# Performance work log

Measured on AMD Instinct MI355X. Metric: run time of the kernel, lower is better.

The kernel has to match this reference:

```python
import jax, jax.numpy as jnp
import numpy as np

B, L, DIM = 16, 4096, 512
N_FFT, HOP, WIN = 1024, 256, 1024
PAD = (WIN - HOP) // 2  # 'same' padding trim
OUT_DIM = N_FFT + 2


def hann_window(win):
    n = jnp.arange(win, dtype=jnp.float32)
    return 0.5 - 0.5 * jnp.cos(2.0 * jnp.pi * n / win)


def setup_inputs() -> dict:
    key = jax.random.key(0)
    k1, k2 = jax.random.split(key)
    x = jax.random.normal(k1, (B, L, DIM), dtype=jnp.float32)
    W = jax.random.normal(k2, (OUT_DIM, DIM), dtype=jnp.float32) * 0.02
    b = jnp.zeros((OUT_DIM,), dtype=jnp.float32)
    return {"x": x, "W": W, "b": b}


def _istft(S):
    # S: (B, N_FFT//2+1, T) complex rfft spectrum
    T = S.shape[-1]
    frames = jnp.fft.irfft(S, n=N_FFT, axis=1)
    window = hann_window(WIN)
    frames = frames * window[None, :, None]
    out_len = (T - 1) * HOP + WIN
    idx = jnp.arange(T)[:, None] * HOP + jnp.arange(WIN)[None, :]
    fr = frames.transpose(0, 2, 1)
    y = jnp.zeros((fr.shape[0], out_len), fr.dtype).at[:, idx].add(fr)
    env = jnp.zeros((out_len,), fr.dtype).at[idx].add(
        jnp.broadcast_to(window * window, idx.shape))
    y = y[:, PAD:out_len - PAD]
    env = env[PAD:out_len - PAD]
    return y / env


def reference(x, W, b):
    # Linear projection: (B, L, DIM) -> (B, L, N_FFT+2)
    h = jnp.einsum('bld,od->blo', x, W) + b
    h = h.transpose(0, 2, 1)                              # (B, N_FFT+2, L)
    mag, p = jnp.split(h, 2, axis=1)                      # each (B, N_FFT//2+1, L)
    mag = jnp.minimum(jnp.exp(mag), 100.0)                # exp + clip(max=100)
    S = mag * jax.lax.complex(jnp.cos(p), jnp.sin(p))
    return _istft(S)                                      # (B, L*HOP)
```

## Files before the change

kernel.cpp:

```cpp
#include <hip/hip_runtime.h>
#include <hip/hip_bf16.h>
#include <math.h>

#define BATCH   16
#define TFRM    4096
#define DIM     512
#define NFFT    1024
#define HOP     256
#define PADC    384
#define MROWS   (BATCH*TFRM)
#define OUTLEN  1048576
#define TWO_PI_OVER_N 0.006135923151542565f
#define INV_TWO_PI    0.15915494309189535f

typedef __bf16 bf16x8 __attribute__((ext_vector_type(8)));
typedef float  f32x4  __attribute__((ext_vector_type(4)));

__device__ __forceinline__ ushort f2bf(float f) {
  union { float f; unsigned u; } v; v.f = f;
  unsigned u = v.u;
  unsigned r = (u + 0x7FFFu + ((u >> 16) & 1u)) >> 16;
  return (ushort)r;
}
__device__ __forceinline__ float bf2f(ushort h) {
  union { unsigned u; float f; } v; v.u = ((unsigned)h) << 16;
  return v.f;
}
__device__ __forceinline__ float fast_sin(float x) { return __builtin_amdgcn_sinf(x * INV_TWO_PI); }
__device__ __forceinline__ float fast_cos(float x) { return __builtin_amdgcn_cosf(x * INV_TWO_PI); }
__device__ __forceinline__ float fast_exp(float x) { return __builtin_amdgcn_exp2f(x * 1.4426950408889634f); }

#define BAR() do { asm volatile("" ::: "memory"); __builtin_amdgcn_s_barrier(); \
                   asm volatile("" ::: "memory"); } while (0)

__global__ void k_prep_x(const float* __restrict__ x, const float* __restrict__ W,
                         const float* __restrict__ bias,
                         ushort* __restrict__ xbf, float* __restrict__ s512) {
  const int row  = blockIdx.x * 4 + (threadIdx.x >> 6);
  const int lane = threadIdx.x & 63;
  const float* xr = x + (size_t)row * DIM + lane * 8;
  float4 v0 = *(const float4*)xr;
  float4 v1 = *(const float4*)(xr + 4);
  ushort4 u0, u1;
  u0.x = f2bf(v0.x); u0.y = f2bf(v0.y); u0.z = f2bf(v0.z); u0.w = f2bf(v0.w);
  u1.x = f2bf(v1.x); u1.y = f2bf(v1.y); u1.z = f2bf(v1.z); u1.w = f2bf(v1.w);
  ushort* xo = xbf + (size_t)row * DIM + lane * 8;
  *(ushort4*)xo = u0;
  *(ushort4*)(xo + 4) = u1;
  const float* w0 = W + 512 * DIM + lane * 8;
  const float* w1 = W + 1025 * DIM + lane * 8;
  float4 a0 = *(const float4*)w0, a1 = *(const float4*)(w0 + 4);
  float4 b0 = *(const float4*)w1, b1 = *(const float4*)(w1 + 4);
  float sm = v0.x*a0.x + v0.y*a0.y + v0.z*a0.z + v0.w*a0.w
           + v1.x*a1.x + v1.y*a1.y + v1.z*a1.z + v1.w*a1.w;
  float sp = v0.x*b0.x + v0.y*b0.y + v0.z*b0.z + v0.w*b0.w
           + v1.x*b1.x + v1.y*b1.y + v1.z*b1.z + v1.w*b1.w;
#pragma unroll
  for (int off = 32; off; off >>= 1) {
    sm += __shfl_down(sm, off);
    sp += __shfl_down(sp, off);
  }
  if (lane == 0) {
    float mag = fminf(fast_exp(sm + bias[512]), 100.0f);
    s512[row] = mag * fast_cos(sp + bias[1025]) * (1.0f / 1024.0f);
  }
}

__global__ void k_prep_w(const float* __restrict__ W, ushort* __restrict__ o) {
  int i = blockIdx.x * 256 + threadIdx.x;
  int r = i >> 9;
  int c = i & 511;
  int orig = (r >> 1) + (r & 1) * 513;
  o[i] = f2bf(W[orig * DIM + c]);
}

__global__ void k_basis(ushort* __restrict__ basE, ushort* __restrict__ basO) {
  int r = blockIdx.x;
  int n = r + 1;
  for (int k = threadIdx.x; k < 512; k += 256) {
    float e, o;
    if (k == 0) { e = 1.0f / 1024.0f; o = 0.0f; }
    else {
      int ph = (k * n) & 1023;
      float ang = (float)ph * TWO_PI_OVER_N;
      e = 2.0f * cosf(ang) * (1.0f / 1024.0f);
      o = 2.0f * sinf(ang) * (1.0f / 1024.0f);
    }
    basE[r * 512 + k] = f2bf(e);
    basO[r * 512 + k] = f2bf(o);
  }
}

template<int EPI>
__global__ __launch_bounds__(512, 2) void k_gemm(const ushort* A, const ushort* A2, int lda,
                                                 const ushort* Bt, const ushort* Bt2, int ldb,
                                                 ushort* C, ushort* C2, int ldc,
                                                 int nbn, int NK, int nsplit,
                                                 const float* __restrict__ bias) {
  __shared__ ushort lds[4][2][8192];
  const int tid  = threadIdx.x;
  const int cpx  = gridDim.x >> 3;
  int bid = (blockIdx.x & 7) * cpx + (blockIdx.x >> 3);
  if (nsplit > 0 && bid >= nsplit) { A = A2; Bt = Bt2; C = C2; bid -= nsplit; }
  const int bm   = bid / nbn;
  const int bn   = bid - bm * nbn;
  const int lane = tid & 63;
  const int wv   = tid >> 6;
  const int wr   = (wv >> 2) * 128;
  const int wc   = (wv & 3) * 64;
  const int fr   = lane & 15;
  const int gq   = lane >> 4;

  const int swz  = ((tid & 3) ^ ((tid >> 3) & 3)) << 3;
  const ushort* gA0 = A  + (size_t)(bm * 256 + (tid >> 2)) * lda + swz;
  const ushort* gA1 = gA0 + (size_t)128 * lda;
  const ushort* gB0 = Bt + (size_t)(bn * 256 + (tid >> 2)) * ldb + swz;
  const ushort* gB1 = gB0 + (size_t)128 * ldb;
  const int lofs = (tid & 448) * 8;

  auto stageA = [&](int S) {
    ushort* d = &lds[S & 3][0][0];
    __builtin_amdgcn_global_load_lds((const __attribute__((address_space(1))) void*)(gA0 + S * 32),
        (__attribute__((address_space(3))) void*)(d + lofs), 16, 0, 0);
    __builtin_amdgcn_global_load_lds((const __attribute__((address_space(1))) void*)(gA1 + S * 32),
        (__attribute__((address_space(3))) void*)(d + 4096 + lofs), 16, 0, 0);
  };
  auto stageB = [&](int S) {
    ushort* d = &lds[S & 3][1][0];
    __builtin_amdgcn_global_load_lds((const __attribute__((address_space(1))) void*)(gB0 + S * 32),
        (__attribute__((address_space(3))) void*)(d + lofs), 16, 0, 0);
    __builtin_amdgcn_global_load_lds((const __attribute__((address_space(1))) void*)(gB1 + S * 32),
        (__attribute__((address_space(3))) void*)(d + 4096 + lofs), 16, 0, 0);
  };
  auto frag = [&](const ushort* lb, int row) -> bf16x8 {
    return *(const bf16x8*)(lb + row * 32 + ((gq ^ ((row >> 1) & 3)) << 3));
  };

  f32x4 acc[8][4] = {};
  bf16x8 bF[4];

  auto phase = [&](int t, int mq, int stg, bool stgA, int wn) {
    const ushort* lA = &lds[t & 3][0][0];
    const ushort* lB = &lds[t & 3][1][0];
    bf16x8 aQ[4];
#pragma unroll
    for (int m = 0; m < 4; ++m) aQ[m] = frag(lA, wr + mq * 64 + m * 16 + fr);
    if (mq == 0) {
#pragma unroll
      for (int n = 0; n < 4; ++n) bF[n] = frag(lB, wc + n * 16 + fr);
    }
    if (stg >= 0) { if (stgA) stageA(stg); else stageB(stg); }
    BAR();
    asm volatile("s_waitcnt lgkmcnt(0)" ::: "memory");
    __builtin_amdgcn_s_setprio(1);
#pragma unroll
    for (int m = 0; m < 4; ++m)
#pragma unroll
      for (int n = 0; n < 4; ++n)
        acc[mq * 4 + m][n] =
            __builtin_amdgcn_mfma_f32_16x16x32_bf16(aQ[m], bF[n], acc[mq * 4 + m][n], 0, 0, 0);
    __builtin_amdgcn_s_setprio(0);
    if (wn == 8)      asm volatile("s_waitcnt vmcnt(8)" ::: "memory");
    else if (wn == 4) asm volatile("s_waitcnt vmcnt(4)" ::: "memory");
    else if (wn == 0) asm volatile("s_waitcnt vmcnt(0)" ::: "memory");
    BAR();
  };

  stageA(0); stageB(0); stageA(1); stageB(1); stageA(2); stageB(2);
  asm volatile("s_waitcnt vmcnt(8)" ::: "memory");
  BAR();

  const int NIT = NK >> 1;
  int j = 0;
  for (; j < NIT - 2; ++j) {
    const int u = 2 * j;
    phase(u,     0, u + 3, true,  -1);
    phase(u,     1, u + 3, false,  8);
    phase(u + 1, 0, u + 4, true,  -1);
    phase(u + 1, 1, u + 4, false,  8);
  }
  {
    const int u = 2 * j;
    phase(u,     0, u + 3, true,  -1);
    phase(u,     1, u + 3, false,  8);
    phase(u + 1, 0, -1,    true,  -1);
    phase(u + 1, 1, -1,    false,  4);
    ++j;
  }
  {
    const int u = 2 * j;
    phase(u,     0, -1, true,  -1);
    phase(u,     1, -1, false,  0);
    phase(u + 1, 0, -1, true,  -1);
    phase(u + 1, 1, -1, false, -1);
  }

  const int r0 = bm * 256 + wr + (gq << 2);
  const int c0 = bn * 256 + wc + fr;
#pragma unroll
  for (int m = 0; m < 8; ++m) {
    if constexpr (EPI == 0) {
#pragma unroll
      for (int j2 = 0; j2 < 4; ++j2) {
        size_t ro = (size_t)(r0 + m * 16 + j2) * ldc + c0;
#pragma unroll
        for (int n = 0; n < 4; ++n)
          C[ro + n * 16] = f2bf(acc[m][n][j2]);
      }
    } else {
#pragma unroll
      for (int n = 0; n < 4; ++n) {
        const int col = c0 + n * 16;
        const int kk  = col >> 1;
        const bool isPhase = (col & 1);
        const float bs = bias[isPhase ? 513 + kk : kk];
        ushort* dst = (isPhase ? C2 : C);
#pragma unroll
        for (int j2 = 0; j2 < 4; ++j2) {
          float v = acc[m][n][j2] + bs;
          float pv = __shfl_xor(v, 1);
          float hm = isPhase ? pv : v;
          float hp = isPhase ? v : pv;
          float mag = fminf(fast_exp(hm), 100.0f);
          float outv = isPhase ? mag * fast_sin(hp) : mag * fast_cos(hp);
          dst[(size_t)(r0 + m * 16 + j2) * ldc + kk] = f2bf(outv);
        }
      }
    }
  }
}

__global__ void k_oa(const ushort* __restrict__ E, const ushort* __restrict__ O,
                     const float* __restrict__ s512, float* __restrict__ out) {
  int u = blockIdx.x * 256 + threadIdx.x;
  int b  = u >> 20;
  int sp = u & (OUTLEN - 1);
  int s  = sp + PADC;
  int t0 = s >> 8;
  int nb = s & 255;
  float acc = 0.0f;
  bool interior = (t0 >= 3) && (t0 < TFRM);
  float env = interior ? 1.5f : 0.0f;
#pragma unroll
  for (int q = 0; q < 4; ++q) {
    int t = t0 - q;
    if (t >= 0 && t < TFRM) {
      int n = nb + (q << 8);
      float w = 0.5f - 0.5f * __builtin_amdgcn_cosf((float)n * (1.0f / 1024.0f));
      if (!interior) env += w * w;
      if (n > 0) {
        size_t base = (((size_t)(b << 12) + t) << 9);
        float sv = s512[(b << 12) + t];
        float par = (n & 1) ? -sv : sv;
        float d;
        if (n <= 512) {
          int idx = n - 1;
          d = bf2f(E[base + idx]) - bf2f(O[base + idx]) + par;
        } else {
          int idx = 1023 - n;
          d = bf2f(E[base + idx]) + bf2f(O[base + idx]) + par;
        }
        acc += w * d;
      }
    }
  }
  out[u] = acc / env;
}

extern "C" void kernel_launch(void* const* d_in, const int* in_sizes, int n_in,
                              void* d_out, int out_size, void* d_ws, size_t ws_size,
                              hipStream_t stream) {
  const float* x    = (const float*)d_in[0];
  const float* W    = (const float*)d_in[1];
  const float* bias = (const float*)d_in[2];
  float* out = (float*)d_out;
  char* ws = (char*)d_ws;

  ushort* xbf  = (ushort*)(ws + 0);
  ushort* Ebuf = (ushort*)(ws + 0);
  ushort* h_a  = (ushort*)(ws + 67108864);
  ushort* h_b  = (ushort*)(ws + 134217728);
  ushort* Obuf = (ushort*)(ws + 201326592);
  ushort* Wp   = (ushort*)(ws + 268435456);
  ushort* basE = (ushort*)(ws + 269484032);
  ushort* basO = (ushort*)(ws + 270008320);
  float*  s512 = (float*) (ws + 270532608);

  k_prep_x<<<MROWS / 4, 256, 0, stream>>>(x, W, bias, xbf, s512);
  k_prep_w<<<(1024 * 512) / 256, 256, 0, stream>>>(W, Wp);
  k_basis<<<512, 256, 0, stream>>>(basE, basO);

  k_gemm<1><<<1024, 512, 0, stream>>>(xbf, nullptr, DIM, Wp, nullptr, DIM,
                                      h_a, h_b, 512, 4, 16, 0, bias);

  k_gemm<0><<<1024, 512, 0, stream>>>(h_a, h_b, 512, basE, basO, 512,
                                      Ebuf, Obuf, 512, 2, 16, 512, nullptr);

  k_oa<<<(BATCH * OUTLEN) / 256, 256, 0, stream>>>(Ebuf, Obuf, s512, out);
}
```

Before: 330.8 us.

## Shrink GEMM tiles to 128x128 double-buffer, fold Nyquist term into GEMM, vectorize overlap-add

Replaces the 256x256 four-stage pipelined GEMM (512 threads, phased MFMA schedule with setprio) with a simpler 128x128 tile, 256-thread, double-buffered loop that syncs every K step. The second GEMM epilogue now adds the Nyquist/parity term from s512 and writes into a padded row stride (520) shifted by one column, so the overlap-add kernel no longer reads s512. The overlap-add kernel handles four output samples per thread with ushort4 loads and float4 stores. The simpler GEMM loses the deeper prefetch and larger tile reuse, which may cost MFMA throughput. In exchange it gains more blocks and simpler indexing.

Result: faster. 314.0 us (-5.1%).

```diff
diff --git a/kernel.cpp b/kernel.cpp
--- a/kernel.cpp
+++ b/kernel.cpp
@@ -10,6 +10,7 @@
 #define PADC    384
 #define MROWS   (BATCH*TFRM)
 #define OUTLEN  1048576
+#define ESTR    520
 #define TWO_PI_OVER_N 0.006135923151542565f
 #define INV_TWO_PI    0.15915494309189535f
 
@@ -29,9 +30,6 @@
 __device__ __forceinline__ float fast_sin(float x) { return __builtin_amdgcn_sinf(x * INV_TWO_PI); }
 __device__ __forceinline__ float fast_cos(float x) { return __builtin_amdgcn_cosf(x * INV_TWO_PI); }
 __device__ __forceinline__ float fast_exp(float x) { return __builtin_amdgcn_exp2f(x * 1.4426950408889634f); }
-
-#define BAR() do { asm volatile("" ::: "memory"); __builtin_amdgcn_s_barrier(); \
-                   asm volatile("" ::: "memory"); } while (0)
 
 __global__ void k_prep_x(const float* __restrict__ x, const float* __restrict__ W,
                          const float* __restrict__ bias,
@@ -92,120 +90,88 @@
 }
 
 template<int EPI>
-__global__ __launch_bounds__(512, 2) void k_gemm(const ushort* A, const ushort* A2, int lda,
-                                                 const ushort* Bt, const ushort* Bt2, int ldb,
-                                                 ushort* C, ushort* C2, int ldc,
-                                                 int nbn, int NK, int nsplit,
-                                                 const float* __restrict__ bias) {
-  __shared__ ushort lds[4][2][8192];
+__global__ __launch_bounds__(256) void k_gemm(const ushort* A, const ushort* A2, int lda,
+                                              const ushort* Bt, const ushort* Bt2, int ldb,
+                                              ushort* C, ushort* C2, int ldc,
+                                              int nbn, int NK, int nsplit,
+                                              const float* __restrict__ bias,
+                                              const float* __restrict__ s512) {
+  __shared__ __align__(16) ushort lds[2][2][128 * 32];
   const int tid  = threadIdx.x;
   const int cpx  = gridDim.x >> 3;
-  int bid = (blockIdx.x & 7) * cpx + (blockIdx.x >> 3);
-  if (nsplit > 0 && bid >= nsplit) { A = A2; Bt = Bt2; C = C2; bid -= nsplit; }
+  int bid  = (blockIdx.x & 7) * cpx + (blockIdx.x >> 3);
+  bool second = false;
+  if (nsplit > 0 && bid >= nsplit) { second = true; A = A2; Bt = Bt2; C = C2; bid -= nsplit; }
   const int bm   = bid / nbn;
   const int bn   = bid - bm * nbn;
   const int lane = tid & 63;
   const int wv   = tid >> 6;
-  const int wr   = (wv >> 2) * 128;
-  const int wc   = (wv & 3) * 64;
-  const int fr   = lane & 15;
-  const int gq   = lane >> 4;
-
-  const int swz  = ((tid & 3) ^ ((tid >> 3) & 3)) << 3;
-  const ushort* gA0 = A  + (size_t)(bm * 256 + (tid >> 2)) * lda + swz;
-  const ushort* gA1 = gA0 + (size_t)128 * lda;
-  const ushort* gB0 = Bt + (size_t)(bn * 256 + (tid >> 2)) * ldb + swz;
-  const ushort* gB1 = gB0 + (size_t)128 * ldb;
-  const int lofs = (tid & 448) * 8;
-
-  auto stageA = [&](int S) {
-    ushort* d = &lds[S & 3][0][0];
-    __builtin_amdgcn_global_load_lds((const __attribute__((address_space(1))) void*)(gA0 + S * 32),
-        (__attribute__((address_space(3))) void*)(d + lofs), 16, 0, 0);
-    __builtin_amdgcn_global_load_lds((const __attribute__((address_space(1))) void*)(gA1 + S * 32),
-        (__attribute__((address_space(3))) void*)(d + 4096 + lofs), 16, 0, 0);
+  const int wr   = (wv >> 1) * 64;
+  const int wc   = (wv & 1) * 64;
+  const int lr   = lane & 15;
+  const int gx   = ((lane >> 4) ^ (lane & 3)) << 3;
+
+  f32x4 acc[4][4] = {};
+
+  const int swz = ((tid & 3) ^ ((tid >> 2) & 3)) << 3;
+  auto stage = [&](const ushort* __restrict__ g, int ld, int row0, int k0, ushort* l) {
+#pragma unroll
+    for (int p = 0; p < 2; ++p) {
+      int i = tid + p * 256;
+      const ushort* gp = g + (size_t)(row0 + (i >> 2)) * ld + k0 + swz;
+      ushort* lp = l + ((i >> 6) << 9);
+      __builtin_amdgcn_global_load_lds(
+          (const __attribute__((address_space(1))) void*)gp,
+          (__attribute__((address_space(3))) void*)lp, 16, 0, 0);
+    }
   };
-  auto stageB = [&](int S) {
-    ushort* d = &lds[S & 3][1][0];
-    __builtin_amdgcn_global_load_lds((const __attribute__((address_space(1))) void*)(gB0 + S * 32),
-        (__attribute__((address_space(3))) void*)(d + lofs), 16, 0, 0);
-    __builtin_amdgcn_global_load_lds((const __attribute__((address_space(1))) void*)(gB1 + S * 32),
-        (__attribute__((address_space(3))) void*)(d + 4096 + lofs), 16, 0, 0);
-  };
-  auto frag = [&](const ushort* lb, int row) -> bf16x8 {
-    return *(const bf16x8*)(lb + row * 32 + ((gq ^ ((row >> 1) & 3)) << 3));
-  };
-
-  f32x4 acc[8][4] = {};
-  bf16x8 bF[4];
-
-  auto phase = [&](int t, int mq, int stg, bool stgA, int wn) {
-    const ushort* lA = &lds[t & 3][0][0];
-    const ushort* lB = &lds[t & 3][1][0];
-    bf16x8 aQ[4];
-#pragma unroll
-    for (int m = 0; m < 4; ++m) aQ[m] = frag(lA, wr + mq * 64 + m * 16 + fr);
-    if (mq == 0) {
-#pragma unroll
-      for (int n = 0; n < 4; ++n) bF[n] = frag(lB, wc + n * 16 + fr);
-    }
-    if (stg >= 0) { if (stgA) stageA(stg); else stageB(stg); }
-    BAR();
-    asm volatile("s_waitcnt lgkmcnt(0)" ::: "memory");
-    __builtin_amdgcn_s_setprio(1);
+
+  stage(A,  lda, bm * 128, 0, &lds[0][0][0]);
+  stage(Bt, ldb, bn * 128, 0, &lds[0][1][0]);
+  asm volatile("s_waitcnt vmcnt(0)" ::: "memory");
+  __syncthreads();
+
+  for (int t = 0; t < NK; ++t) {
+    const int cur = t & 1;
+    if (t + 1 < NK) {
+      stage(A,  lda, bm * 128, (t + 1) << 5, &lds[cur ^ 1][0][0]);
+      stage(Bt, ldb, bn * 128, (t + 1) << 5, &lds[cur ^ 1][1][0]);
+    }
+    const ushort* lA = &lds[cur][0][0];
+    const ushort* lB = &lds[cur][1][0];
+    bf16x8 aF[4], bF[4];
 #pragma unroll
     for (int m = 0; m < 4; ++m)
+      aF[m] = *(const bf16x8*)(lA + (wr + m * 16 + lr) * 32 + gx);
+#pragma unroll
+    for (int n = 0; n < 4; ++n)
+      bF[n] = *(const bf16x8*)(lB + (wc + n * 16 + lr) * 32 + gx);
+#pragma unroll
+    for (int m = 0; m < 4; ++m)
 #pragma unroll
       for (int n = 0; n < 4; ++n)
-        acc[mq * 4 + m][n] =
-            __builtin_amdgcn_mfma_f32_16x16x32_bf16(aQ[m], bF[n], acc[mq * 4 + m][n], 0, 0, 0);
-    __builtin_amdgcn_s_setprio(0);
-    if (wn == 8)      asm volatile("s_waitcnt vmcnt(8)" ::: "memory");
-    else if (wn == 4) asm volatile("s_waitcnt vmcnt(4)" ::: "memory");
-    else if (wn == 0) asm volatile("s_waitcnt vmcnt(0)" ::: "memory");
-    BAR();
-  };
-
-  stageA(0); stageB(0); stageA(1); stageB(1); stageA(2); stageB(2);
-  asm volatile("s_waitcnt vmcnt(8)" ::: "memory");
-  BAR();
-
-  const int NIT = NK >> 1;
-  int j = 0;
-  for (; j < NIT - 2; ++j) {
-    const int u = 2 * j;
-    phase(u,     0, u + 3, true,  -1);
-    phase(u,     1, u + 3, false,  8);
-    phase(u + 1, 0, u + 4, true,  -1);
-    phase(u + 1, 1, u + 4, false,  8);
-  }
-  {
-    const int u = 2 * j;
-    phase(u,     0, u + 3, true,  -1);
-    phase(u,     1, u + 3, false,  8);
-    phase(u + 1, 0, -1,    true,  -1);
-    phase(u + 1, 1, -1,    false,  4);
-    ++j;
-  }
-  {
-    const int u = 2 * j;
-    phase(u,     0, -1, true,  -1);
-    phase(u,     1, -1, false,  0);
-    phase(u + 1, 0, -1, true,  -1);
-    phase(u + 1, 1, -1, false, -1);
-  }
-
-  const int r0 = bm * 256 + wr + (gq << 2);
-  const int c0 = bn * 256 + wc + fr;
-#pragma unroll
-  for (int m = 0; m < 8; ++m) {
+        acc[m][n] = __builtin_amdgcn_mfma_f32_16x16x32_bf16(aF[m], bF[n], acc[m][n], 0, 0, 0);
+    asm volatile("s_waitcnt vmcnt(0)" ::: "memory");
+    __syncthreads();
+  }
+
+  const int r0 = bm * 128 + wr + ((lane >> 4) << 2);
+  const int c0 = bn * 128 + wc + lr;
+#pragma unroll
+  for (int m = 0; m < 4; ++m) {
     if constexpr (EPI == 0) {
-#pragma unroll
-      for (int j2 = 0; j2 < 4; ++j2) {
-        size_t ro = (size_t)(r0 + m * 16 + j2) * ldc + c0;
-#pragma unroll
-        for (int n = 0; n < 4; ++n)
-          C[ro + n * 16] = f2bf(acc[m][n][j2]);
+      float4 sv4 = {0.f, 0.f, 0.f, 0.f};
+      if (!second) sv4 = *(const float4*)(s512 + r0 + m * 16);
+#pragma unroll
+      for (int j = 0; j < 4; ++j) {
+        size_t ro = (size_t)(r0 + m * 16 + j) * ldc;
+        float sv = ((const float*)&sv4)[j];
+#pragma unroll
+        for (int n = 0; n < 4; ++n) {
+          int c = c0 + n * 16;
+          float par = second ? 0.0f : ((c & 1) ? sv : -sv);
+          C[ro + c + 1] = f2bf(acc[m][n][j] + par);
+        }
       }
     } else {
 #pragma unroll
@@ -216,14 +182,14 @@
         const float bs = bias[isPhase ? 513 + kk : kk];
         ushort* dst = (isPhase ? C2 : C);
 #pragma unroll
-        for (int j2 = 0; j2 < 4; ++j2) {
-          float v = acc[m][n][j2] + bs;
+        for (int j = 0; j < 4; ++j) {
+          float v = acc[m][n][j] + bs;
           float pv = __shfl_xor(v, 1);
           float hm = isPhase ? pv : v;
           float hp = isPhase ? v : pv;
           float mag = fminf(fast_exp(hm), 100.0f);
           float outv = isPhase ? mag * fast_sin(hp) : mag * fast_cos(hp);
-          dst[(size_t)(r0 + m * 16 + j2) * ldc + kk] = f2bf(outv);
+          dst[(size_t)(r0 + m * 16 + j) * ldc + kk] = f2bf(outv);
         }
       }
     }
@@ -231,40 +197,57 @@
 }
 
 __global__ void k_oa(const ushort* __restrict__ E, const ushort* __restrict__ O,
-                     const float* __restrict__ s512, float* __restrict__ out) {
+                     float* __restrict__ out) {
   int u = blockIdx.x * 256 + threadIdx.x;
-  int b  = u >> 20;
-  int sp = u & (OUTLEN - 1);
-  int s  = sp + PADC;
+  int b  = u >> 18;
+  int g  = u & 262143;
+  int s  = (g << 2) + PADC;
   int t0 = s >> 8;
   int nb = s & 255;
-  float acc = 0.0f;
+  float acc[4] = {0.f, 0.f, 0.f, 0.f};
   bool interior = (t0 >= 3) && (t0 < TFRM);
-  float env = interior ? 1.5f : 0.0f;
+  float env[4];
+#pragma unroll
+  for (int j = 0; j < 4; ++j) env[j] = interior ? 1.5f : 0.0f;
 #pragma unroll
   for (int q = 0; q < 4; ++q) {
     int t = t0 - q;
-    if (t >= 0 && t < TFRM) {
-      int n = nb + (q << 8);
-      float w = 0.5f - 0.5f * __builtin_amdgcn_cosf((float)n * (1.0f / 1024.0f));
-      if (!interior) env += w * w;
-      if (n > 0) {
-        size_t base = (((size_t)(b << 12) + t) << 9);
-        float sv = s512[(b << 12) + t];
-        float par = (n & 1) ? -sv : sv;
-        float d;
-        if (n <= 512) {
-          int idx = n - 1;
-          d = bf2f(E[base + idx]) - bf2f(O[base + idx]) + par;
-        } else {
-          int idx = 1023 - n;
-          d = bf2f(E[base + idx]) + bf2f(O[base + idx]) + par;
-        }
-        acc += w * d;
-      }
-    }
-  }
-  out[u] = acc / env;
+    if (t < 0 || t >= TFRM) continue;
+    int n = nb + (q << 8);
+    size_t base = ((size_t)(b << 12) + t) * ESTR;
+    float w[4];
+#pragma unroll
+    for (int j = 0; j < 4; ++j) {
+      w[j] = 0.5f - 0.5f * __builtin_amdgcn_cosf((float)(n + j) * (1.0f / 1024.0f));
+      if (!interior) env[j] += w[j] * w[j];
+    }
+    float d[4];
+    if (n + 3 <= 512) {
+      ushort4 e = *(const ushort4*)(E + base + n);
+      ushort4 o = *(const ushort4*)(O + base + n);
+      d[0] = bf2f(e.x) - bf2f(o.x); d[1] = bf2f(e.y) - bf2f(o.y);
+      d[2] = bf2f(e.z) - bf2f(o.z); d[3] = bf2f(e.w) - bf2f(o.w);
+    } else if (n >= 516) {
+      int m2 = 1024 - n;
+      ushort4 e0 = *(const ushort4*)(E + base + m2);
+      ushort4 e1 = *(const ushort4*)(E + base + m2 - 4);
+      ushort4 o0 = *(const ushort4*)(O + base + m2);
+      ushort4 o1 = *(const ushort4*)(O + base + m2 - 4);
+      d[0] = bf2f(e0.x) + bf2f(o0.x); d[1] = bf2f(e1.w) + bf2f(o1.w);
+      d[2] = bf2f(e1.z) + bf2f(o1.z); d[3] = bf2f(e1.y) + bf2f(o1.y);
+    } else {
+      d[0] = bf2f(E[base + 512]) - bf2f(O[base + 512]);
+      d[1] = bf2f(E[base + 511]) + bf2f(O[base + 511]);
+      d[2] = bf2f(E[base + 510]) + bf2f(O[base + 510]);
+      d[3] = bf2f(E[base + 509]) + bf2f(O[base + 509]);
+    }
+#pragma unroll
+    for (int j = 0; j < 4; ++j) acc[j] += w[j] * d[j];
+  }
+  float4 o4;
+  o4.x = acc[0] / env[0]; o4.y = acc[1] / env[1];
+  o4.z = acc[2] / env[2]; o4.w = acc[3] / env[3];
+  *(float4*)(out + (size_t)u * 4) = o4;
 }
 
 extern "C" void kernel_launch(void* const* d_in, const int* in_sizes, int n_in,
@@ -277,24 +260,25 @@
   char* ws = (char*)d_ws;
 
   ushort* xbf  = (ushort*)(ws + 0);
-  ushort* Ebuf = (ushort*)(ws + 0);
-  ushort* h_a  = (ushort*)(ws + 67108864);
-  ushort* h_b  = (ushort*)(ws + 134217728);
-  ushort* Obuf = (ushort*)(ws + 201326592);
-  ushort* Wp   = (ushort*)(ws + 268435456);
-  ushort* basE = (ushort*)(ws + 269484032);
-  ushort* basO = (ushort*)(ws + 270008320);
-  float*  s512 = (float*) (ws + 270532608);
+  ushort* Epp  = (ushort*)(ws + 0);
+  ushort* h_a  = (ushort*)(ws + 68157440);
+  ushort* h_b  = (ushort*)(ws + 135266304);
+  ushort* Obuf = (ushort*)(ws + 202375168);
+  ushort* Wp   = (ushort*)(ws + 270532608);
+  ushort* basE = (ushort*)(ws + 271581184);
+  ushort* basO = (ushort*)(ws + 272105472);
+  float*  s512 = (float*) (ws + 272629760);
 
   k_prep_x<<<MROWS / 4, 256, 0, stream>>>(x, W, bias, xbf, s512);
   k_prep_w<<<(1024 * 512) / 256, 256, 0, stream>>>(W, Wp);
   k_basis<<<512, 256, 0, stream>>>(basE, basO);
 
-  k_gemm<1><<<1024, 512, 0, stream>>>(xbf, nullptr, DIM, Wp, nullptr, DIM,
-                                      h_a, h_b, 512, 4, 16, 0, bias);
-
-  k_gemm<0><<<1024, 512, 0, stream>>>(h_a, h_b, 512, basE, basO, 512,
-                                      Ebuf, Obuf, 512, 2, 16, 512, nullptr);
-
-  k_oa<<<(BATCH * OUTLEN) / 256, 256, 0, stream>>>(Ebuf, Obuf, s512, out);
-}
+  k_gemm<1><<<(MROWS / 128) * 8, 256, 0, stream>>>(
+      xbf, nullptr, DIM, Wp, nullptr, DIM, h_a, h_b, 512, 8, 16, 0, bias, nullptr);
+
+  k_gemm<0><<<2 * (MROWS / 128) * 4, 256, 0, stream>>>(
+      h_a, h_b, 512, basE, basO, 512, Epp, Obuf, ESTR, 4, 16, (MROWS / 128) * 4,
+      nullptr, s512);
+
+  k_oa<<<(BATCH * OUTLEN) / 1024, 256, 0, stream>>>(Epp, Obuf, out);
+}
```
